# Performance work log

Measured on AMD Instinct MI355X. Metric: run time of the kernel, lower is better.

Reference implementation:

```python
import jax, jax.numpy as jnp
import numpy as np

D_K = 128
SCALER = np.sqrt(D_K).astype(np.float32)

def setup_inputs() -> dict:
    key = jax.random.key(0)
    kq, kk, kv = jax.random.split(key, 3)
    B, L, D = 16, 2048, D_K
    q = jax.random.normal(kq, (B, L, D), dtype=jnp.float32)
    k = jax.random.normal(kk, (B, L, D), dtype=jnp.float32)
    v = jax.random.normal(kv, (B, L, D), dtype=jnp.float32)
    return {"q": q, "k": k, "v": v}

def reference(q, k, v):
    # score[b, i, j] = q[b, i, :] . k[b, j, :] / sqrt(d_k)
    score = jnp.einsum('bid,bjd->bij', q, k) / SCALER
    attn = jax.nn.softmax(score, axis=-1)
    # output[b, i, :] = sum_j attn[b, i, j] * v[b, j, :]
    return jnp.einsum('bij,bjd->bid', attn, v)
```

## Files before the change

### kernel.cpp

```cpp
#include <hip/hip_runtime.h>
#include <stdint.h>


typedef short bf16x8 __attribute__((ext_vector_type(8)));
typedef float f32x4 __attribute__((ext_vector_type(4)));
typedef unsigned int u32;
typedef unsigned short u16;

#define L_SEQ  2048
#define D_HEAD 128
#define TSZ    8388608u
#define W_PART (2u * TSZ)
#define W_LSUM (W_PART + 512u * 32768u)
#define WS_NEED (W_LSUM + 512u * 256u * 4u)

__device__ __forceinline__ unsigned pk2(float lo, float hi) {
    union { float f; unsigned u; } a, b;
    a.f = lo; b.f = hi;
    return __builtin_amdgcn_perm(b.u + 0x8000u, a.u + 0x8000u, 0x07060302u);
}
__device__ __forceinline__ float ex2(float x) { return __builtin_amdgcn_exp2f(x); }
__device__ __forceinline__ float bflo(unsigned w) {
    union { unsigned u; float f; } v; v.u = w << 16; return v.f;
}
__device__ __forceinline__ float bfhi(unsigned w) {
    union { unsigned u; float f; } v; v.u = w & 0xffff0000u; return v.f;
}
__device__ __forceinline__ void gl_lds16(const u16* g, u16* l) {
    __builtin_amdgcn_global_load_lds(
        (const __attribute__((address_space(1))) u32*)g,
        (__attribute__((address_space(3))) u32*)l, 16, 0, 0);
}

__global__ __launch_bounds__(256, 4)
void prepass(const float* __restrict__ K, const float* __restrict__ V,
             u16* __restrict__ kb, u16* __restrict__ vt) {
    const int id = blockIdx.x, t = threadIdx.x;
    if (id < 512) {
        const float* src = K + (size_t)id * 64 * 128;
        u16*        dst = kb + (size_t)id * 64 * 128;
        const int r = t >> 2;
        #pragma unroll
        for (int i = 0; i < 4; ++i) {
            int gp = (t & 3) * 4 + i;
            int gs = gp ^ (r & 7);
            const float* s = src + r * 128 + gs * 8;
            float4 x0 = *(const float4*)s, x1 = *(const float4*)(s + 4);
            uint4 w;
            w.x = pk2(x0.x, x0.y); w.y = pk2(x0.z, x0.w);
            w.z = pk2(x1.x, x1.y); w.w = pk2(x1.z, x1.w);
            *(uint4*)(dst + r * 128 + gp * 8) = w;
        }
    } else {
        __shared__ __align__(16) u16 vl[128 * 72];
        const int bid = id - 512;
        const float* src = V + (size_t)bid * 64 * 128;
        const int vcc = t & 31, vgk = t >> 5;
        union { float4 v; float f[4]; } vr[8];
        const float* vp = src + (size_t)(vgk * 8) * 128 + vcc * 4;
        #pragma unroll
        for (int r = 0; r < 8; ++r) vr[r].v = *(const float4*)(vp + (size_t)r * 128);
        #pragma unroll
        for (int dd = 0; dd < 4; ++dd) {
            uint4 w;
            w.x = pk2(vr[0].f[dd], vr[1].f[dd]);
            w.y = pk2(vr[2].f[dd], vr[3].f[dd]);
            w.z = pk2(vr[4].f[dd], vr[5].f[dd]);
            w.w = pk2(vr[6].f[dd], vr[7].f[dd]);
            *(uint4*)(&vl[(vcc * 4 + dd) * 72 + vgk * 8]) = w;
        }
        __syncthreads();
        u16* dst = vt + (size_t)bid * 8192;
        #pragma unroll
        for (int i = 0; i < 4; ++i) {
            int flat = t + 256 * i;
            int d = flat >> 3, gp = flat & 7;
            uint4 w = *(const uint4*)(&vl[d * 72 + ((gp ^ (d & 7)) * 8)]);
            *(uint4*)(dst + (size_t)flat * 8) = w;
        }
    }
}

__global__ __launch_bounds__(512, 4)
void attnD(const float* __restrict__ Qg, const u16* __restrict__ kb,
           const u16* __restrict__ vt, u16* __restrict__ part,
           float* __restrict__ lsum) {
    __shared__ __align__(16) char smem[49152];
    const int tid = threadIdx.x;
    const int wv = tid >> 6, lane = tid & 63;
    const int c = lane & 15, qd = lane >> 4, cx = c & 7;
    const int qs = wv >> 1, dh = wv & 1;
    const int bid = blockIdx.x;
    const int kvh = bid >> 8, p = bid & 255;
    const int b = p & 15, qblk = p >> 4;
    const int nt = 16;

    const float* Qp = Qg + (size_t)b * L_SEQ * D_HEAD;
    const u16*   Kp = kb + (size_t)b * L_SEQ * D_HEAD + (size_t)kvh * 16 * 8192;
    const u16*   Vp = vt + (size_t)b * 32 * 8192 + (size_t)kvh * 16 * 8192;
    u16* Kl = (u16*)smem;
    u16* Vl = (u16*)(smem + 16384);
    u16* Pq = (u16*)(smem + 32768) + qs * 2048;
    const int psw = cx << 1;
    const int so = tid * 8;

    gl_lds16(Kp + so, Kl + so);
    gl_lds16(Kp + so + 4096, Kl + so + 4096);
    gl_lds16(Vp + so, Vl + so);
    gl_lds16(Vp + so + 4096, Vl + so + 4096);

    const float QS = 1.4426950408889634f / 11.313708498984761f;
    bf16x8 qf[2][4];
    #pragma unroll
    for (int s = 0; s < 2; ++s) {
        const float* qrow = Qp + (size_t)(qblk * 128 + qs * 32 + s * 16 + c) * 128 + qd * 8;
        #pragma unroll
        for (int kt = 0; kt < 4; ++kt) {
            float4 x0 = *(const float4*)(qrow + kt * 32);
            float4 x1 = *(const float4*)(qrow + kt * 32 + 4);
            union { unsigned u[4]; bf16x8 v; } tt;
            tt.u[0] = pk2(x0.x * QS, x0.y * QS);
            tt.u[1] = pk2(x0.z * QS, x0.w * QS);
            tt.u[2] = pk2(x1.x * QS, x1.y * QS);
            tt.u[3] = pk2(x1.z * QS, x1.w * QS);
            qf[s][kt] = tt.v;
        }
    }

    f32x4 acc[2][4];
    #pragma unroll
    for (int s = 0; s < 2; ++s)
        #pragma unroll
        for (int dt = 0; dt < 4; ++dt) acc[s][dt] = (f32x4){0.f, 0.f, 0.f, 0.f};
    float lrun[2] = {0.f, 0.f};

    __syncthreads();

    for (int it = 0; it < nt; ++it) {
        f32x4 st[2][2];
        #pragma unroll
        for (int v = 0; v < 2; ++v) {
            st[v][0] = (f32x4){0.f, 0.f, 0.f, 0.f};
            st[v][1] = (f32x4){0.f, 0.f, 0.f, 0.f};
        }
        #pragma unroll
        for (int kt = 0; kt < 4; ++kt) {
            const int g = ((kt * 4 + qd) ^ cx) * 8;
            #pragma unroll
            for (int v = 0; v < 2; ++v) {
                bf16x8 a = *(const bf16x8*)(Kl + (dh * 32 + v * 16 + c) * 128 + g);
                st[v][0] = __builtin_amdgcn_mfma_f32_16x16x32_bf16(a, qf[0][kt], st[v][0], 0, 0, 0);
                st[v][1] = __builtin_amdgcn_mfma_f32_16x16x32_bf16(a, qf[1][kt], st[v][1], 0, 0, 0);
            }
        }

        #pragma unroll
        for (int s = 0; s < 2; ++s) {
            float lsm = 0.f;
            #pragma unroll
            for (int v = 0; v < 2; ++v) {
                float p0 = ex2(st[v][s].x), p1 = ex2(st[v][s].y);
                float p2 = ex2(st[v][s].z), p3 = ex2(st[v][s].w);
                lsm += (p0 + p1) + (p2 + p3);
                uint2 w; w.x = pk2(p0, p1); w.y = pk2(p2, p3);
                int gsw = (dh * 8 + v * 4 + qd) ^ psw;
                *(uint2*)(Pq + (s * 16 + c) * 64 + gsw * 4) = w;
            }
            lrun[s] += lsm;
        }
        __syncthreads();

        if (it + 1 < nt) {
            const u16* kg = Kp + (size_t)(it + 1) * 8192 + so;
            gl_lds16(kg, Kl + so);
            gl_lds16(kg + 4096, Kl + so + 4096);
        }

        bf16x8 pf[2][2];
        #pragma unroll
        for (int h = 0; h < 2; ++h) {
            int gsw = (h * 8 + qd * 2) ^ psw;
            #pragma unroll
            for (int s = 0; s < 2; ++s)
                pf[h][s] = *(const bf16x8*)(Pq + (s * 16 + c) * 64 + gsw * 4);
        }
        #pragma unroll
        for (int dt = 0; dt < 4; ++dt) {
            #pragma unroll
            for (int h = 0; h < 2; ++h) {
                bf16x8 av = *(const bf16x8*)(Vl + (dh * 64 + dt * 16 + c) * 64
                                                + ((h * 4 + qd) ^ cx) * 8);
                acc[0][dt] = __builtin_amdgcn_mfma_f32_16x16x32_bf16(av, pf[h][0], acc[0][dt], 0, 0, 0);
                acc[1][dt] = __builtin_amdgcn_mfma_f32_16x16x32_bf16(av, pf[h][1], acc[1][dt], 0, 0, 0);
            }
        }

        if (it + 1 < nt) {
            __syncthreads();
            const u16* vg = Vp + (size_t)(it + 1) * 8192 + so;
            gl_lds16(vg, Vl + so);
            gl_lds16(vg + 4096, Vl + so + 4096);
        }
    }

    float ls[2];
    #pragma unroll
    for (int s = 0; s < 2; ++s) {
        float l = lrun[s];
        l += __shfl_xor(l, 16);
        l += __shfl_xor(l, 32);
        ls[s] = l;
    }
    u16* pb = part + (size_t)bid * 16384;
    #pragma unroll
    for (int s = 0; s < 2; ++s)
        #pragma unroll
        for (int dt = 0; dt < 4; ++dt) {
            f32x4 o = acc[s][dt];
            uint2 w; w.x = pk2(o.x, o.y); w.y = pk2(o.z, o.w);
            *(uint2*)(pb + ((((((qs * 2 + dh) * 2 + s) * 4 + dt) * 64) + lane) << 2)) = w;
        }
    if (qd == 0) {
        lsum[(size_t)bid * 256 + dh * 128 + qs * 32 + c]      = ls[0];
        lsum[(size_t)bid * 256 + dh * 128 + qs * 32 + 16 + c] = ls[1];
    }
}

__global__ __launch_bounds__(256, 2)
void combineD(const u16* __restrict__ part, const float* __restrict__ lsum,
              float* __restrict__ Og) {
    __shared__ float inv[128];
    __shared__ __align__(16) float Ol[64 * 132];
    const int t = threadIdx.x, p = blockIdx.x;
    const int b = p & 15, qblk = p >> 4;
    if (t < 128) {
        float l = 0.f;
        #pragma unroll
        for (int kvh = 0; kvh < 2; ++kvh)
            #pragma unroll
            for (int dh = 0; dh < 2; ++dh)
                l += lsum[(size_t)(kvh * 256 + p) * 256 + dh * 128 + t];
        inv[t] = 1.0f / l;
    }
    const uint2* S0 = (const uint2*)(part + (size_t)p * 16384);
    const uint2* S1 = (const uint2*)(part + (size_t)(256 + p) * 16384);
    __syncthreads();
    #pragma unroll
    for (int h2 = 0; h2 < 2; ++h2) {
        #pragma unroll
        for (int i = 0; i < 8; ++i) {
            int slot = i * 256 + t;
            int qs_l = slot >> 10;
            int rem  = slot & 1023;
            int dh = rem >> 9, s = (rem >> 8) & 1;
            int dt = (rem >> 6) & 3, lane = rem & 63;
            int qd = lane >> 4, cc = lane & 15;
            int qs = h2 * 2 + qs_l;
            int rowl = qs_l * 32 + s * 16 + cc;
            int row  = h2 * 64 + rowl;
            int d0 = dh * 64 + dt * 16 + qd * 4;
            size_t idx = (size_t)((((qs * 2 + dh) * 2 + s) * 4 + dt) * 64 + lane);
            uint2 w0 = S0[idx], w1 = S1[idx];
            float iv = inv[row];
            float4 o;
            o.x = (bflo(w0.x) + bflo(w1.x)) * iv;
            o.y = (bfhi(w0.x) + bfhi(w1.x)) * iv;
            o.z = (bflo(w0.y) + bflo(w1.y)) * iv;
            o.w = (bfhi(w0.y) + bfhi(w1.y)) * iv;
            *(float4*)(&Ol[rowl * 132 + d0]) = o;
        }
        __syncthreads();
        #pragma unroll
        for (int i = 0; i < 8; ++i) {
            int slot = i * 256 + t;
            int row = slot >> 5, c4 = slot & 31;
            float4 val = *(const float4*)(&Ol[row * 132 + c4 * 4]);
            size_t q = (size_t)b * L_SEQ + qblk * 128 + h2 * 64 + row;
            *(float4*)(Og + q * D_HEAD + c4 * 4) = val;
        }
        __syncthreads();
    }
}

extern "C" void kernel_launch(void* const* d_in, const int* in_sizes, int n_in,
                              void* d_out, int out_size, void* d_ws, size_t ws_size,
                              hipStream_t stream) {
    const float* q = (const float*)d_in[0];
    const float* k = (const float*)d_in[1];
    const float* v = (const float*)d_in[2];
    float* out = (float*)d_out;
    u16* kb = (u16*)d_ws;
    u16* vt = (u16*)((char*)d_ws + TSZ);
    u16* part = (u16*)((char*)d_ws + W_PART);
    float* ls = (float*)((char*)d_ws + W_LSUM);
    prepass<<<dim3(1024), dim3(256), 0, stream>>>(k, v, kb, vt);
    attnD<<<dim3(512), dim3(512), 0, stream>>>(q, kb, vt, part, ls);
    combineD<<<dim3(256), dim3(256), 0, stream>>>(part, ls, out);
}
```

Baseline: 136.6 us.

## Switch attention to 32x32 MFMA with register-resident P via permlane swap

Rewrites the attention kernel to use 32x32x16 bf16 MFMA, with each wave owning 32 query rows across the full head dimension. Previously each wave split head dimension with another wave. The softmax probabilities are packed with v_cvt_pk_bf16_f32 and rearranged in registers with v_permlane32_swap, so the P tile no longer goes through LDS. Block size drops to 256 threads and LDS to 32KB, and the combine kernel and lsum layout are adjusted to match. This removes LDS traffic and one sync stage for P, but raises accumulator register pressure and halves the waves per block.

```diff
diff --git a/kernel.cpp b/kernel.cpp
--- a/kernel.cpp
+++ b/kernel.cpp
@@ -4,6 +4,7 @@
 
 typedef short bf16x8 __attribute__((ext_vector_type(8)));
 typedef float f32x4 __attribute__((ext_vector_type(4)));
+typedef float f32x16 __attribute__((ext_vector_type(16)));
 typedef unsigned int u32;
 typedef unsigned short u16;
 
@@ -12,7 +13,7 @@
 #define TSZ    8388608u
 #define W_PART (2u * TSZ)
 #define W_LSUM (W_PART + 512u * 32768u)
-#define WS_NEED (W_LSUM + 512u * 256u * 4u)
+#define WS_NEED (W_LSUM + 512u * 128u * 4u)
 
 __device__ __forceinline__ unsigned pk2(float lo, float hi) {
     union { float f; unsigned u; } a, b;
@@ -25,6 +26,14 @@
 }
 __device__ __forceinline__ float bfhi(unsigned w) {
     union { unsigned u; float f; } v; v.u = w & 0xffff0000u; return v.f;
+}
+__device__ __forceinline__ u32 cvtpk(float lo, float hi) {
+    u32 d;
+    asm("v_cvt_pk_bf16_f32 %0, %1, %2" : "=v"(d) : "v"(lo), "v"(hi));
+    return d;
+}
+__device__ __forceinline__ void plswap(u32& a, u32& b) {
+    asm volatile("v_permlane32_swap_b32 %0, %1" : "+v"(a), "+v"(b));
 }
 __device__ __forceinline__ void gl_lds16(const u16* g, u16* l) {
     __builtin_amdgcn_global_load_lds(
@@ -81,15 +90,14 @@
     }
 }
 
-__global__ __launch_bounds__(512, 4)
-void attnD(const float* __restrict__ Qg, const u16* __restrict__ kb,
+__global__ __launch_bounds__(256, 2)
+void attnR(const float* __restrict__ Qg, const u16* __restrict__ kb,
            const u16* __restrict__ vt, u16* __restrict__ part,
            float* __restrict__ lsum) {
-    __shared__ __align__(16) char smem[49152];
+    __shared__ __align__(16) char smem[32768];
     const int tid = threadIdx.x;
-    const int wv = tid >> 6, lane = tid & 63;
-    const int c = lane & 15, qd = lane >> 4, cx = c & 7;
-    const int qs = wv >> 1, dh = wv & 1;
+    const int qs = tid >> 6, lane = tid & 63;
+    const int q32 = lane & 31, hi = lane >> 5;
     const int bid = blockIdx.x;
     const int kvh = bid >> 8, p = bid & 255;
     const int b = p & 15, qblk = p >> 4;
@@ -100,174 +108,156 @@
     const u16*   Vp = vt + (size_t)b * 32 * 8192 + (size_t)kvh * 16 * 8192;
     u16* Kl = (u16*)smem;
     u16* Vl = (u16*)(smem + 16384);
-    u16* Pq = (u16*)(smem + 32768) + qs * 2048;
-    const int psw = cx << 1;
-    const int so = tid * 8;
-
-    gl_lds16(Kp + so, Kl + so);
-    gl_lds16(Kp + so + 4096, Kl + so + 4096);
-    gl_lds16(Vp + so, Vl + so);
-    gl_lds16(Vp + so + 4096, Vl + so + 4096);
+    const int so = qs * 2048 + lane * 8;
+
+    #pragma unroll
+    for (int i = 0; i < 4; ++i) {
+        gl_lds16(Kp + so + i * 512, Kl + so + i * 512);
+        gl_lds16(Vp + so + i * 512, Vl + so + i * 512);
+    }
 
     const float QS = 1.4426950408889634f / 11.313708498984761f;
-    bf16x8 qf[2][4];
-    #pragma unroll
-    for (int s = 0; s < 2; ++s) {
-        const float* qrow = Qp + (size_t)(qblk * 128 + qs * 32 + s * 16 + c) * 128 + qd * 8;
-        #pragma unroll
-        for (int kt = 0; kt < 4; ++kt) {
-            float4 x0 = *(const float4*)(qrow + kt * 32);
-            float4 x1 = *(const float4*)(qrow + kt * 32 + 4);
-            union { unsigned u[4]; bf16x8 v; } tt;
+    bf16x8 qf[8];
+    {
+        const float* qrow = Qp + (size_t)(qblk * 128 + qs * 32 + q32) * 128 + hi * 8;
+        #pragma unroll
+        for (int s8 = 0; s8 < 8; ++s8) {
+            float4 x0 = *(const float4*)(qrow + s8 * 16);
+            float4 x1 = *(const float4*)(qrow + s8 * 16 + 4);
+            union { u32 u[4]; bf16x8 v; } tt;
             tt.u[0] = pk2(x0.x * QS, x0.y * QS);
             tt.u[1] = pk2(x0.z * QS, x0.w * QS);
             tt.u[2] = pk2(x1.x * QS, x1.y * QS);
             tt.u[3] = pk2(x1.z * QS, x1.w * QS);
-            qf[s][kt] = tt.v;
-        }
-    }
-
-    f32x4 acc[2][4];
-    #pragma unroll
-    for (int s = 0; s < 2; ++s)
-        #pragma unroll
-        for (int dt = 0; dt < 4; ++dt) acc[s][dt] = (f32x4){0.f, 0.f, 0.f, 0.f};
-    float lrun[2] = {0.f, 0.f};
+            qf[s8] = tt.v;
+        }
+    }
+
+    f32x16 acc[4];
+    #pragma unroll
+    for (int dt = 0; dt < 4; ++dt)
+        acc[dt] = (f32x16){0.f,0.f,0.f,0.f,0.f,0.f,0.f,0.f,
+                           0.f,0.f,0.f,0.f,0.f,0.f,0.f,0.f};
+    float lrun = 0.f;
 
     __syncthreads();
 
     for (int it = 0; it < nt; ++it) {
-        f32x4 st[2][2];
-        #pragma unroll
-        for (int v = 0; v < 2; ++v) {
-            st[v][0] = (f32x4){0.f, 0.f, 0.f, 0.f};
-            st[v][1] = (f32x4){0.f, 0.f, 0.f, 0.f};
-        }
-        #pragma unroll
-        for (int kt = 0; kt < 4; ++kt) {
-            const int g = ((kt * 4 + qd) ^ cx) * 8;
-            #pragma unroll
-            for (int v = 0; v < 2; ++v) {
-                bf16x8 a = *(const bf16x8*)(Kl + (dh * 32 + v * 16 + c) * 128 + g);
-                st[v][0] = __builtin_amdgcn_mfma_f32_16x16x32_bf16(a, qf[0][kt], st[v][0], 0, 0, 0);
-                st[v][1] = __builtin_amdgcn_mfma_f32_16x16x32_bf16(a, qf[1][kt], st[v][1], 0, 0, 0);
-            }
-        }
-
-        #pragma unroll
-        for (int s = 0; s < 2; ++s) {
-            float lsm = 0.f;
-            #pragma unroll
-            for (int v = 0; v < 2; ++v) {
-                float p0 = ex2(st[v][s].x), p1 = ex2(st[v][s].y);
-                float p2 = ex2(st[v][s].z), p3 = ex2(st[v][s].w);
-                lsm += (p0 + p1) + (p2 + p3);
-                uint2 w; w.x = pk2(p0, p1); w.y = pk2(p2, p3);
-                int gsw = (dh * 8 + v * 4 + qd) ^ psw;
-                *(uint2*)(Pq + (s * 16 + c) * 64 + gsw * 4) = w;
-            }
-            lrun[s] += lsm;
+        f32x16 st0 = (f32x16){0.f,0.f,0.f,0.f,0.f,0.f,0.f,0.f,
+                              0.f,0.f,0.f,0.f,0.f,0.f,0.f,0.f};
+        f32x16 st1 = st0;
+        const int lx = q32 & 7;
+        #pragma unroll
+        for (int s8 = 0; s8 < 8; ++s8) {
+            const int gs = ((s8 * 2 + hi) ^ lx) * 8;
+            bf16x8 a0 = *(const bf16x8*)(Kl + q32 * 128 + gs);
+            bf16x8 a1 = *(const bf16x8*)(Kl + (32 + q32) * 128 + gs);
+            st0 = __builtin_amdgcn_mfma_f32_32x32x16_bf16(a0, qf[s8], st0, 0, 0, 0);
+            st1 = __builtin_amdgcn_mfma_f32_32x32x16_bf16(a1, qf[s8], st1, 0, 0, 0);
         }
         __syncthreads();
 
         if (it + 1 < nt) {
             const u16* kg = Kp + (size_t)(it + 1) * 8192 + so;
-            gl_lds16(kg, Kl + so);
-            gl_lds16(kg + 4096, Kl + so + 4096);
-        }
-
-        bf16x8 pf[2][2];
-        #pragma unroll
-        for (int h = 0; h < 2; ++h) {
-            int gsw = (h * 8 + qd * 2) ^ psw;
-            #pragma unroll
-            for (int s = 0; s < 2; ++s)
-                pf[h][s] = *(const bf16x8*)(Pq + (s * 16 + c) * 64 + gsw * 4);
-        }
+            #pragma unroll
+            for (int i = 0; i < 4; ++i) gl_lds16(kg + i * 512, Kl + so + i * 512);
+        }
+
+        bf16x8 pf[4];
+        #pragma unroll
+        for (int v = 0; v < 2; ++v) {
+            float pp[16];
+            #pragma unroll
+            for (int e = 0; e < 16; ++e) {
+                float sv = (v == 0) ? st0[e] : st1[e];
+                pp[e] = ex2(sv);
+                lrun += pp[e];
+            }
+            u32 wa0 = cvtpk(pp[0], pp[1]),  wb0 = cvtpk(pp[4], pp[5]);
+            u32 wa1 = cvtpk(pp[2], pp[3]),  wb1 = cvtpk(pp[6], pp[7]);
+            plswap(wa0, wb0); plswap(wa1, wb1);
+            u32 wc0 = cvtpk(pp[8], pp[9]),  wd0 = cvtpk(pp[12], pp[13]);
+            u32 wc1 = cvtpk(pp[10], pp[11]), wd1 = cvtpk(pp[14], pp[15]);
+            plswap(wc0, wd0); plswap(wc1, wd1);
+            union { u32 u[4]; bf16x8 x; } t0, t1;
+            t0.u[0] = wa0; t0.u[1] = wa1; t0.u[2] = wb0; t0.u[3] = wb1;
+            t1.u[0] = wc0; t1.u[1] = wc1; t1.u[2] = wd0; t1.u[3] = wd1;
+            pf[v * 2]     = t0.x;
+            pf[v * 2 + 1] = t1.x;
+        }
+
         #pragma unroll
         for (int dt = 0; dt < 4; ++dt) {
-            #pragma unroll
-            for (int h = 0; h < 2; ++h) {
-                bf16x8 av = *(const bf16x8*)(Vl + (dh * 64 + dt * 16 + c) * 64
-                                                + ((h * 4 + qd) ^ cx) * 8);
-                acc[0][dt] = __builtin_amdgcn_mfma_f32_16x16x32_bf16(av, pf[h][0], acc[0][dt], 0, 0, 0);
-                acc[1][dt] = __builtin_amdgcn_mfma_f32_16x16x32_bf16(av, pf[h][1], acc[1][dt], 0, 0, 0);
+            const int R = dt * 32 + q32;
+            const int rx = R & 7;
+            #pragma unroll
+            for (int ks = 0; ks < 4; ++ks) {
+                bf16x8 av = *(const bf16x8*)(Vl + R * 64 + ((ks * 2 + hi) ^ rx) * 8);
+                acc[dt] = __builtin_amdgcn_mfma_f32_32x32x16_bf16(av, pf[ks], acc[dt], 0, 0, 0);
             }
         }
+        __syncthreads();
 
         if (it + 1 < nt) {
-            __syncthreads();
             const u16* vg = Vp + (size_t)(it + 1) * 8192 + so;
-            gl_lds16(vg, Vl + so);
-            gl_lds16(vg + 4096, Vl + so + 4096);
-        }
-    }
-
-    float ls[2];
-    #pragma unroll
-    for (int s = 0; s < 2; ++s) {
-        float l = lrun[s];
-        l += __shfl_xor(l, 16);
-        l += __shfl_xor(l, 32);
-        ls[s] = l;
-    }
-    u16* pb = part + (size_t)bid * 16384;
-    #pragma unroll
-    for (int s = 0; s < 2; ++s)
-        #pragma unroll
-        for (int dt = 0; dt < 4; ++dt) {
-            f32x4 o = acc[s][dt];
-            uint2 w; w.x = pk2(o.x, o.y); w.y = pk2(o.z, o.w);
-            *(uint2*)(pb + ((((((qs * 2 + dh) * 2 + s) * 4 + dt) * 64) + lane) << 2)) = w;
-        }
-    if (qd == 0) {
-        lsum[(size_t)bid * 256 + dh * 128 + qs * 32 + c]      = ls[0];
-        lsum[(size_t)bid * 256 + dh * 128 + qs * 32 + 16 + c] = ls[1];
-    }
+            #pragma unroll
+            for (int i = 0; i < 4; ++i) gl_lds16(vg + i * 512, Vl + so + i * 512);
+        }
+    }
+
+    float l = lrun + __shfl_xor(lrun, 32);
+    uint2* pw = (uint2*)(part + (size_t)bid * 16384);
+    #pragma unroll
+    for (int dt = 0; dt < 4; ++dt) {
+        f32x16 o = acc[dt];
+        #pragma unroll
+        for (int jj = 0; jj < 4; ++jj) {
+            uint2 w;
+            w.x = pk2(o[jj * 4 + 0], o[jj * 4 + 1]);
+            w.y = pk2(o[jj * 4 + 2], o[jj * 4 + 3]);
+            pw[(((qs * 4 + dt) * 4 + jj) << 6) + lane] = w;
+        }
+    }
+    if (lane < 32)
+        lsum[(size_t)bid * 128 + qs * 32 + lane] = l;
 }
 
 __global__ __launch_bounds__(256, 2)
-void combineD(const u16* __restrict__ part, const float* __restrict__ lsum,
+void combineR(const u16* __restrict__ part, const float* __restrict__ lsum,
               float* __restrict__ Og) {
     __shared__ float inv[128];
     __shared__ __align__(16) float Ol[64 * 132];
     const int t = threadIdx.x, p = blockIdx.x;
     const int b = p & 15, qblk = p >> 4;
     if (t < 128) {
-        float l = 0.f;
-        #pragma unroll
-        for (int kvh = 0; kvh < 2; ++kvh)
-            #pragma unroll
-            for (int dh = 0; dh < 2; ++dh)
-                l += lsum[(size_t)(kvh * 256 + p) * 256 + dh * 128 + t];
+        float l = lsum[(size_t)p * 128 + t] + lsum[(size_t)(256 + p) * 128 + t];
         inv[t] = 1.0f / l;
     }
     const uint2* S0 = (const uint2*)(part + (size_t)p * 16384);
     const uint2* S1 = (const uint2*)(part + (size_t)(256 + p) * 16384);
     __syncthreads();
     #pragma unroll
-    for (int h2 = 0; h2 < 2; ++h2) {
+    for (int h = 0; h < 2; ++h) {
         #pragma unroll
         for (int i = 0; i < 8; ++i) {
             int slot = i * 256 + t;
             int qs_l = slot >> 10;
-            int rem  = slot & 1023;
-            int dh = rem >> 9, s = (rem >> 8) & 1;
-            int dt = (rem >> 6) & 3, lane = rem & 63;
-            int qd = lane >> 4, cc = lane & 15;
-            int qs = h2 * 2 + qs_l;
-            int rowl = qs_l * 32 + s * 16 + cc;
-            int row  = h2 * 64 + rowl;
-            int d0 = dh * 64 + dt * 16 + qd * 4;
-            size_t idx = (size_t)((((qs * 2 + dh) * 2 + s) * 4 + dt) * 64 + lane);
+            int dt   = (slot >> 8) & 3;
+            int jj   = (slot >> 6) & 3;
+            int lane = slot & 63;
+            int hi = lane >> 5, q32 = lane & 31;
+            int qs = h * 2 + qs_l;
+            int row_l = qs_l * 32 + q32;
+            int d0 = dt * 32 + hi * 4 + jj * 8;
+            size_t idx = (size_t)(((qs * 4 + dt) * 4 + jj) << 6) + lane;
             uint2 w0 = S0[idx], w1 = S1[idx];
-            float iv = inv[row];
+            float iv = inv[h * 64 + row_l];
             float4 o;
             o.x = (bflo(w0.x) + bflo(w1.x)) * iv;
             o.y = (bfhi(w0.x) + bfhi(w1.x)) * iv;
             o.z = (bflo(w0.y) + bflo(w1.y)) * iv;
             o.w = (bfhi(w0.y) + bfhi(w1.y)) * iv;
-            *(float4*)(&Ol[rowl * 132 + d0]) = o;
+            *(float4*)(&Ol[row_l * 132 + d0]) = o;
         }
         __syncthreads();
         #pragma unroll
@@ -275,7 +265,7 @@
             int slot = i * 256 + t;
             int row = slot >> 5, c4 = slot & 31;
             float4 val = *(const float4*)(&Ol[row * 132 + c4 * 4]);
-            size_t q = (size_t)b * L_SEQ + qblk * 128 + h2 * 64 + row;
+            size_t q = (size_t)b * L_SEQ + qblk * 128 + h * 64 + row;
             *(float4*)(Og + q * D_HEAD + c4 * 4) = val;
         }
         __syncthreads();
@@ -294,6 +284,6 @@
     u16* part = (u16*)((char*)d_ws + W_PART);
     float* ls = (float*)((char*)d_ws + W_LSUM);
     prepass<<<dim3(1024), dim3(256), 0, stream>>>(k, v, kb, vt);
-    attnD<<<dim3(512), dim3(512), 0, stream>>>(q, kb, vt, part, ls);
-    combineD<<<dim3(256), dim3(256), 0, stream>>>(part, ls, out);
-}
+    attnR<<<dim3(512), dim3(256), 0, stream>>>(q, kb, vt, part, ls);
+    combineR<<<dim3(256), dim3(256), 0, stream>>>(part, ls, out);
+}
```

New measurement: 136.2 us. Within noise of the previous version (-0.3%).
